# Kernel optimization log

Hardware: AMD Instinct MI355X
Metric: run time of the kernel (lower is better)

Reference implementation:

```python
import jax, jax.numpy as jnp
import numpy as np

B, S, H = 2, 2048, 2048
NH, DH = 16, 128
T, L = 8, 64
FF = 4 * H
SCALE = DH ** -0.5
EPS = 1e-5


def _ln(x, g, b):
    m = jnp.mean(x, axis=-1, keepdims=True)
    v = jnp.mean(jnp.square(x - m), axis=-1, keepdims=True)
    return (x - m) * jax.lax.rsqrt(v + EPS) * g + b


def setup_inputs() -> dict:
    key = jax.random.key(0)
    ks = jax.random.split(key, 10)
    def w(k, shape):
        return jax.random.normal(k, shape, jnp.float32) * (shape[0] ** -0.5)
    return {
        "hidden_states": jax.random.normal(ks[0], (B, S, H), jnp.float32),
        "image_embeds": jax.random.normal(ks[1], (B, T, L, H), jnp.float32),
        "media_locations": jax.random.randint(ks[2], (B, S), 0, 2).astype(bool),
        "Wq": w(ks[3], (H, NH * DH)),
        "Wk": w(ks[4], (H, NH * DH)),
        "Wv": w(ks[5], (H, NH * DH)),
        "Wo": w(ks[6], (NH * DH, H)),
        "ln_attn_g": jnp.ones((H,), jnp.float32),
        "ln_attn_b": jnp.zeros((H,), jnp.float32),
        "ln_ff_g": jnp.ones((H,), jnp.float32),
        "ln_ff_b": jnp.zeros((H,), jnp.float32),
        "W1": w(ks[7], (H, FF)),
        "b1": jnp.zeros((FF,), jnp.float32),
        "W2": w(ks[8], (FF, H)),
        "b2": jnp.zeros((H,), jnp.float32),
        # nonzero gates so the attention/ffn branches carry gradient signal
        "gamma_attn": jnp.full((1,), 0.1, jnp.float32),
        "gamma_ff": jnp.full((1,), 0.1, jnp.float32),
    }


def reference(hidden_states, image_embeds, media_locations,
              Wq, Wk, Wv, Wo, ln_attn_g, ln_attn_b, ln_ff_g, ln_ff_b,
              W1, b1, W2, b2, gamma_attn, gamma_ff):
    b, s, d = hidden_states.shape
    x = _ln(hidden_states, ln_attn_g, ln_attn_b)
    kv = image_embeds.reshape(b, -1, d)              # [B, T*L, D]
    q = (x @ Wq).reshape(b, s, NH, DH)               # [B, S, H, Dh]
    k = (kv @ Wk).reshape(b, -1, NH, DH)             # [B, KV, H, Dh]
    v = (kv @ Wv).reshape(b, -1, NH, DH)
    scores = jnp.einsum('bqhd,bkhd->bhqk', q, k) * SCALE
    # mask is per query row: rows with media_locations==False are fully masked.
    # Use large-finite neg (not -inf) to avoid NaN rows; those rows are zeroed below anyway.
    neg = jnp.finfo(scores.dtype).min
    scores = jnp.where(media_locations[:, None, :, None], scores, neg)
    attn = jax.nn.softmax(scores, axis=-1)
    out = jnp.einsum('bhqk,bkhd->bqhd', attn, v).reshape(b, s, NH * DH) @ Wo
    gated = jnp.tanh(gamma_attn) * out * media_locations[..., None].astype(hidden_states.dtype)
    x = hidden_states + gated
    ff = jax.nn.gelu(_ln(x, ln_ff_g, ln_ff_b) @ W1 + b1, approximate=False) @ W2 + b2
    return x + jnp.tanh(gamma_ff) * ff
```

## Files before the change

### kernel.cpp

```cpp
#include <hip/hip_runtime.h>
#include <math.h>
#include <stdint.h>

typedef __bf16 bf16;
typedef __bf16 bf16x8 __attribute__((ext_vector_type(8)));
typedef __bf16 bf16x4 __attribute__((ext_vector_type(4)));
typedef float f32x4 __attribute__((ext_vector_type(4)));

#define DEV __device__ __forceinline__

DEV void g2l16(void* lds, const void* g) {
    __builtin_amdgcn_global_load_lds(
        (const __attribute__((address_space(1))) uint32_t*)g,
        (__attribute__((address_space(3))) uint32_t*)lds,
        16, 0, 0);
}

DEV float gelu_fast(float x) {
    float u = -1.5957691216f * __builtin_fmaf(0.044715f * x, x * x, x);
    return x * __builtin_amdgcn_rcpf(1.f + __expf(u));
}

DEV uint8_t to_fp8(float x) {
    return (uint8_t)(__builtin_amdgcn_cvt_pk_fp8_f32(x, x, 0, false) & 0xff);
}

DEV void xcd_swizzle(int& bx, int& by, int& bz) {
    int gx = gridDim.x, gy = gridDim.y, gz = gridDim.z;
    int nwg = gx * gy * gz;
    if (nwg & 7) return;
    long flat = ((long)bz * gy + by) * gx + bx;
    long q = nwg >> 3;
    long sw = (flat & 7) * q + (flat >> 3);
    bx = (int)(sw % gx);
    long t = sw / gx;
    by = (int)(t % gy);
    bz = (int)(t / gy);
}

template <int EPI, typename TC>
__global__ __launch_bounds__(256)
void gemm_bt(const bf16* __restrict__ A, const bf16* __restrict__ Bt, TC* __restrict__ C,
             int K, int lda, int ldb, int ldc,
             long sAo, long sAi, long sBo, long sBi, long sCo, long sCi, int zInner,
             float alpha,
             const float* __restrict__ resid,
             const float* __restrict__ gamma,
             const int* __restrict__ mask)
{
    int bx = blockIdx.x, by = blockIdx.y, bz = blockIdx.z;
    xcd_swizzle(bx, by, bz);

    int zo = bz / zInner, zi = bz % zInner;
    A  += (long)zo * sAo + (long)zi * sAi;
    Bt += (long)zo * sBo + (long)zi * sBi;
    long cOff = (long)zo * sCo + (long)zi * sCi;

    int tileN = bx * 128, tileM = by * 128;

    __shared__ bf16 As[8192];
    __shared__ bf16 Bs[8192];

    int tid = threadIdx.x;
    int wave = tid >> 6, lane = tid & 63, quad = lane >> 4, l15 = lane & 15;
    int wm = (wave >> 1) * 64, wn = (wave & 1) * 64;

    f32x4 acc[4][4] = {};

    for (int k0 = 0; k0 < K; k0 += 64) {
#pragma unroll
        for (int r = 0; r < 4; ++r) {
            int c = r * 256 + tid;
            int kc = c >> 7, row = c & 127;
            g2l16(&As[c * 8], A + (long)(tileM + row) * lda + (k0 + kc * 8));
            g2l16(&Bs[c * 8], Bt + (long)(tileN + row) * ldb + (k0 + kc * 8));
        }
        __syncthreads();
#pragma unroll
        for (int ks = 0; ks < 2; ++ks) {
            bf16x8 af[4], bq[4];
#pragma unroll
            for (int i = 0; i < 4; ++i) {
                af[i] = *(const bf16x8*)&As[((ks * 4 + quad) * 128 + wm + i * 16 + l15) * 8];
                bq[i] = *(const bf16x8*)&Bs[((ks * 4 + quad) * 128 + wn + i * 16 + l15) * 8];
            }
#pragma unroll
            for (int mi = 0; mi < 4; ++mi)
#pragma unroll
                for (int ni = 0; ni < 4; ++ni)
                    acc[mi][ni] = __builtin_amdgcn_mfma_f32_16x16x32_bf16(
                        af[mi], bq[ni], acc[mi][ni], 0, 0, 0);
        }
        __syncthreads();
    }

    float gscale = 0.f;
    if (EPI == 2) gscale = tanhf(gamma[0]);

#pragma unroll
    for (int mi = 0; mi < 4; ++mi) {
#pragma unroll
        for (int r = 0; r < 4; ++r) {
            int gm = tileM + wm + mi * 16 + quad * 4 + r;
            float rowmask = 1.f;
            if (EPI == 2) rowmask = mask[gm] ? 1.f : 0.f;
#pragma unroll
            for (int ni = 0; ni < 4; ++ni) {
                int gn = tileN + wn + ni * 16 + l15;
                float v = acc[mi][ni][r] * alpha;
                float r0;
                if (EPI == 0) {
                    r0 = v;
                } else {
                    float h = resid[(long)gm * ldc + gn];
                    r0 = h + gscale * v * rowmask;
                }
                C[cOff + (long)gm * ldc + gn] = (TC)r0;
            }
        }
    }
}

__global__ __launch_bounds__(256)
void gemm_fp8(const uint8_t* __restrict__ A, const uint8_t* __restrict__ Bt,
              float* __restrict__ C, int K, int lda, int ldb, int ldc, float alpha,
              const float* __restrict__ resid,
              const float* __restrict__ bias,
              const float* __restrict__ gamma)
{
    int bx = blockIdx.x, by = blockIdx.y, bz = blockIdx.z;
    xcd_swizzle(bx, by, bz);

    int tileN = bx * 128, tileM = by * 128;

    __shared__ uint8_t As[16384];
    __shared__ uint8_t Bs[16384];

    int tid = threadIdx.x;
    int wave = tid >> 6, lane = tid & 63, quad = lane >> 4, l15 = lane & 15;
    int wm = (wave >> 1) * 64, wn = (wave & 1) * 64;

    f32x4 acc[4][4] = {};

    for (int k0 = 0; k0 < K; k0 += 128) {
#pragma unroll
        for (int r = 0; r < 4; ++r) {
            int c = r * 256 + tid;
            int kc = c >> 7, row = c & 127;
            g2l16(&As[c * 16], A + (long)(tileM + row) * lda + (k0 + kc * 16));
            g2l16(&Bs[c * 16], Bt + (long)(tileN + row) * ldb + (k0 + kc * 16));
        }
        __syncthreads();
#pragma unroll
        for (int ks = 0; ks < 4; ++ks) {
            int kc16 = ks * 2 + (quad >> 1);
            int boff = (quad & 1) * 8;
            long af[4], bq[4];
#pragma unroll
            for (int i = 0; i < 4; ++i) {
                af[i] = *(const long*)&As[(kc16 * 128 + wm + i * 16 + l15) * 16 + boff];
                bq[i] = *(const long*)&Bs[(kc16 * 128 + wn + i * 16 + l15) * 16 + boff];
            }
#pragma unroll
            for (int mi = 0; mi < 4; ++mi)
#pragma unroll
                for (int ni = 0; ni < 4; ++ni)
                    acc[mi][ni] = __builtin_amdgcn_mfma_f32_16x16x32_fp8_fp8(
                        af[mi], bq[ni], acc[mi][ni], 0, 0, 0);
        }
        __syncthreads();
    }

    float gscale = tanhf(gamma[0]);
    float bb[4];
#pragma unroll
    for (int ni = 0; ni < 4; ++ni)
        bb[ni] = bias[tileN + wn + ni * 16 + l15];

#pragma unroll
    for (int mi = 0; mi < 4; ++mi) {
#pragma unroll
        for (int r = 0; r < 4; ++r) {
            int gm = tileM + wm + mi * 16 + quad * 4 + r;
#pragma unroll
            for (int ni = 0; ni < 4; ++ni) {
                int gn = tileN + wn + ni * 16 + l15;
                float h = resid[(long)gm * ldc + gn];
                C[(long)gm * ldc + gn] = h + gscale * (acc[mi][ni][r] * alpha + bb[ni]);
            }
        }
    }
}

__global__ __launch_bounds__(512, 2)
void gemm256_h1(const bf16* __restrict__ A, const bf16* __restrict__ Bt,
                uint8_t* __restrict__ C, int K, int lda, int ldb, int ldc,
                const float* __restrict__ bias)
{
    __shared__ bf16 lds[3][2][8192];

    int bx = blockIdx.x, by = blockIdx.y, bz = blockIdx.z;
    xcd_swizzle(bx, by, bz);

    int tid = threadIdx.x;
    int wave = tid >> 6, lane = tid & 63, quad = lane >> 4, l15 = lane & 15;
    int wm = (wave >> 2) * 128, wn = (wave & 3) * 64;
    int tileN = bx * 256, tileM = by * 256;

    int c0 = tid, c1 = 512 + tid;
    int kc0 = c0 >> 8, row0 = c0 & 255;
    int kc1 = c1 >> 8, row1 = c1 & 255;
    const bf16* A0 = A + (long)(tileM + row0) * lda + kc0 * 8;
    const bf16* A1 = A + (long)(tileM + row1) * lda + kc1 * 8;
    const bf16* B0 = Bt + (long)(tileN + row0) * ldb + kc0 * 8;
    const bf16* B1 = Bt + (long)(tileN + row1) * ldb + kc1 * 8;

    f32x4 acc[8][4] = {};

    int aoff = (quad * 256 + wm + l15) * 8;
    int boff = (quad * 256 + wn + l15) * 8;

    auto stage = [&](int t, int b) {
        int k0 = t * 32;
        g2l16(&lds[b][0][c0 * 8], A0 + k0);
        g2l16(&lds[b][0][c1 * 8], A1 + k0);
        g2l16(&lds[b][1][c0 * 8], B0 + k0);
        g2l16(&lds[b][1][c1 * 8], B1 + k0);
    };

    stage(0, 0);
    stage(1, 1);

    int T = K >> 5;
    int cb = 0;
    for (int t = 0; t < T; ++t) {
        int nb = cb + 2; if (nb >= 3) nb -= 3;
        stage(t + 2, nb);

        asm volatile("s_waitcnt vmcnt(8)\n\ts_barrier" ::: "memory");

        const bf16* pA = &lds[cb][0][0];
        const bf16* pB = &lds[cb][1][0];
        bf16x8 af[8], bq[4];
#pragma unroll
        for (int mi = 0; mi < 8; ++mi)
            af[mi] = *(const bf16x8*)&pA[aoff + mi * 128];
#pragma unroll
        for (int ni = 0; ni < 4; ++ni)
            bq[ni] = *(const bf16x8*)&pB[boff + ni * 128];

        __builtin_amdgcn_s_setprio(1);
#pragma unroll
        for (int mi = 0; mi < 8; ++mi)
#pragma unroll
            for (int ni = 0; ni < 4; ++ni)
                acc[mi][ni] = __builtin_amdgcn_mfma_f32_16x16x32_bf16(
                    af[mi], bq[ni], acc[mi][ni], 0, 0, 0);
        __builtin_amdgcn_s_setprio(0);

        asm volatile("s_barrier" ::: "memory");
        cb = (cb == 2) ? 0 : cb + 1;
    }

    float bb[4];
#pragma unroll
    for (int ni = 0; ni < 4; ++ni)
        bb[ni] = bias[tileN + wn + ni * 16 + l15];

#pragma unroll
    for (int mi = 0; mi < 8; ++mi) {
#pragma unroll
        for (int r = 0; r < 4; ++r) {
            int gm = tileM + wm + mi * 16 + quad * 4 + r;
#pragma unroll
            for (int ni = 0; ni < 4; ++ni) {
                int gn = tileN + wn + ni * 16 + l15;
                float x = acc[mi][ni][r] + bb[ni];
                C[(long)gm * ldc + gn] = to_fp8(8.f * gelu_fast(x));
            }
        }
    }
}

__global__ __launch_bounds__(256)
void ln_k(const float* __restrict__ x, const float* __restrict__ g, const float* __restrict__ b,
          bf16* __restrict__ out)
{
    long row = blockIdx.x;
    int tid = threadIdx.x;
    int wave = tid >> 6, lane = tid & 63;
    const float* px = x + row * 2048 + tid * 8;

    float4 a = *(const float4*)px;
    float4 c = *(const float4*)(px + 4);
    float f[8] = {a.x, a.y, a.z, a.w, c.x, c.y, c.z, c.w};

    float s = 0.f, s2 = 0.f;
#pragma unroll
    for (int j = 0; j < 8; ++j) { s += f[j]; s2 += f[j] * f[j]; }
    for (int o = 32; o; o >>= 1) { s += __shfl_xor(s, o, 64); s2 += __shfl_xor(s2, o, 64); }

    __shared__ float red[8];
    if (lane == 0) { red[wave] = s; red[4 + wave] = s2; }
    __syncthreads();
    s  = red[0] + red[1] + red[2] + red[3];
    s2 = red[4] + red[5] + red[6] + red[7];

    float mean = s * (1.f / 2048.f);
    float var  = s2 * (1.f / 2048.f) - mean * mean;
    float rstd = rsqrtf(var + 1e-5f);

    int col = tid * 8;
    bf16x8 o8;
#pragma unroll
    for (int j = 0; j < 8; ++j)
        o8[j] = (bf16)((f[j] - mean) * rstd * g[col + j] + b[col + j]);
    *(bf16x8*)(out + row * 2048 + tid * 8) = o8;
}

__global__ __launch_bounds__(256)
void softmax512(bf16* __restrict__ s)
{
    long row = (long)blockIdx.x * 4 + (threadIdx.x >> 6);
    int lane = threadIdx.x & 63;
    bf16* p = s + row * 512 + lane * 8;
    bf16x8 v = *(const bf16x8*)p;
    float f[8], mx = -1e30f;
#pragma unroll
    for (int j = 0; j < 8; ++j) { f[j] = (float)v[j]; mx = fmaxf(mx, f[j]); }
    for (int o = 32; o; o >>= 1) mx = fmaxf(mx, __shfl_xor(mx, o, 64));
    float sum = 0.f;
#pragma unroll
    for (int j = 0; j < 8; ++j) { f[j] = __expf(f[j] - mx); sum += f[j]; }
    for (int o = 32; o; o >>= 1) sum += __shfl_xor(sum, o, 64);
    float r = 1.f / sum;
    bf16x8 o8;
#pragma unroll
    for (int j = 0; j < 8; ++j) o8[j] = (bf16)(f[j] * r);
    *(bf16x8*)p = o8;
}

__global__ __launch_bounds__(256)
void transpose_cvt(const float* __restrict__ in, bf16* __restrict__ out, int ldi, int ldo)
{
    __shared__ float t[64][33];
    int tx = threadIdx.x & 31, ty = threadIdx.x >> 5;
    int n0 = blockIdx.x * 32, m0 = blockIdx.y * 64;
#pragma unroll
    for (int i = 0; i < 8; ++i)
        t[ty + i * 8][tx] = in[(long)(m0 + ty + i * 8) * ldi + n0 + tx];
    __syncthreads();
    int wx = threadIdx.x & 15, wy = threadIdx.x >> 4;
#pragma unroll
    for (int j = 0; j < 2; ++j) {
        int n = wy + j * 16;
        bf16x4 v;
        v[0] = (bf16)t[4 * wx + 0][n];
        v[1] = (bf16)t[4 * wx + 1][n];
        v[2] = (bf16)t[4 * wx + 2][n];
        v[3] = (bf16)t[4 * wx + 3][n];
        *(bf16x4*)(out + (long)(n0 + n) * ldo + m0 + 4 * wx) = v;
    }
}

__global__ __launch_bounds__(256)
void transpose_cvt8(const float* __restrict__ in, uint8_t* __restrict__ out,
                    int ldi, int ldo, float scale)
{
    __shared__ float t[64][33];
    int tx = threadIdx.x & 31, ty = threadIdx.x >> 5;
    int n0 = blockIdx.x * 32, m0 = blockIdx.y * 64;
#pragma unroll
    for (int i = 0; i < 8; ++i)
        t[ty + i * 8][tx] = in[(long)(m0 + ty + i * 8) * ldi + n0 + tx];
    __syncthreads();
    int wx = threadIdx.x & 15, wy = threadIdx.x >> 4;
#pragma unroll
    for (int j = 0; j < 2; ++j) {
        int n = wy + j * 16;
        int p = __builtin_amdgcn_cvt_pk_fp8_f32(
            scale * t[4 * wx + 0][n], scale * t[4 * wx + 1][n], 0, false);
        p = __builtin_amdgcn_cvt_pk_fp8_f32(
            scale * t[4 * wx + 2][n], scale * t[4 * wx + 3][n], p, true);
        *(int*)(out + (long)(n0 + n) * ldo + m0 + 4 * wx) = p;
    }
}

__global__ __launch_bounds__(256)
void transpose_k(const bf16* __restrict__ in, bf16* __restrict__ out,
                 int ldi, int ldo, long sIo, long sIi, long sOo, long sOi, int zInner)
{
    int z = blockIdx.z;
    in  += (long)(z / zInner) * sIo + (long)(z % zInner) * sIi;
    out += (long)(z / zInner) * sOo + (long)(z % zInner) * sOi;
    __shared__ bf16 t[32][33];
    int tx = threadIdx.x & 31, ty = threadIdx.x >> 5;
    int n0 = blockIdx.x * 32, m0 = blockIdx.y * 32;
#pragma unroll
    for (int i = 0; i < 4; ++i)
        t[ty + i * 8][tx] = in[(long)(m0 + ty + i * 8) * ldi + n0 + tx];
    __syncthreads();
#pragma unroll
    for (int i = 0; i < 4; ++i)
        out[(long)(n0 + ty + i * 8) * ldo + m0 + tx] = t[tx][ty + i * 8];
}

__global__ __launch_bounds__(256)
void cvt_k(const float* __restrict__ in, bf16* __restrict__ out)
{
    int i = (blockIdx.x * 256 + threadIdx.x) * 4;
    float4 v = *(const float4*)(in + i);
    out[i + 0] = (bf16)v.x;
    out[i + 1] = (bf16)v.y;
    out[i + 2] = (bf16)v.z;
    out[i + 3] = (bf16)v.w;
}

extern "C" void kernel_launch(void* const* d_in, const int* in_sizes, int n_in,
                              void* d_out, int out_size, void* d_ws, size_t ws_size,
                              hipStream_t stream)
{
    const float* hidden = (const float*)d_in[0];
    const float* image  = (const float*)d_in[1];
    const int*   media  = (const int*)d_in[2];
    const float* Wq = (const float*)d_in[3];
    const float* Wk = (const float*)d_in[4];
    const float* Wv = (const float*)d_in[5];
    const float* Wo = (const float*)d_in[6];
    const float* lag = (const float*)d_in[7];
    const float* lab = (const float*)d_in[8];
    const float* lfg = (const float*)d_in[9];
    const float* lfb = (const float*)d_in[10];
    const float* W1 = (const float*)d_in[11];
    const float* b1 = (const float*)d_in[12];
    const float* W2 = (const float*)d_in[13];
    const float* b2 = (const float*)d_in[14];
    const float* ga = (const float*)d_in[15];
    const float* gf = (const float*)d_in[16];
    float* out = (float*)d_out;

    char* ws = (char*)d_ws;
    const size_t MB = 1ull << 20;
    bf16* WqT  = (bf16*)(ws + 0);
    bf16* WkT  = (bf16*)(ws + 8 * MB);
    bf16* WvT  = (bf16*)(ws + 16 * MB);
    bf16* WoT  = (bf16*)(ws + 24 * MB);
    bf16* W1T  = (bf16*)(ws + 0);
    uint8_t* W2T8 = (uint8_t*)(ws + 32 * MB);
    bf16* xln  = (bf16*)(ws + 32 * MB);
    bf16* q    = (bf16*)(ws + 48 * MB);
    bf16* kbuf = (bf16*)(ws + 64 * MB);
    bf16* vbuf = (bf16*)(ws + 68 * MB);
    bf16* vt   = (bf16*)(ws + 72 * MB);
    bf16* imgb = (bf16*)(ws + 76 * MB);
    bf16* sc   = (bf16*)(ws + 80 * MB);
    uint8_t* h1f8 = (uint8_t*)(ws + 80 * MB);
    float* x2  = (float*)(ws + 144 * MB);

    const float SCALE = 0.08838834764831845f;
    const float A8 = 8.f, B8 = 64.f;
    dim3 blk(256);

    transpose_cvt<<<dim3(64, 32, 1), blk, 0, stream>>>(Wq, WqT, 2048, 2048);
    transpose_cvt<<<dim3(64, 32, 1), blk, 0, stream>>>(Wk, WkT, 2048, 2048);
    transpose_cvt<<<dim3(64, 32, 1), blk, 0, stream>>>(Wv, WvT, 2048, 2048);
    transpose_cvt<<<dim3(64, 32, 1), blk, 0, stream>>>(Wo, WoT, 2048, 2048);
    cvt_k<<<2048, blk, 0, stream>>>(image, imgb);

    ln_k<<<4096, blk, 0, stream>>>(hidden, lag, lab, xln);

    gemm_bt<0, bf16><<<dim3(16, 32, 1), blk, 0, stream>>>(
        xln, WqT, q, 2048, 2048, 2048, 2048, 0, 0, 0, 0, 0, 0, 1, 1.f,
        nullptr, nullptr, nullptr);

    gemm_bt<0, bf16><<<dim3(16, 8, 2), blk, 0, stream>>>(
        imgb, WkT, kbuf, 2048, 2048, 2048, 2048,
        0, 0, 0, 4194304, 0, 2097152, 2, 1.f,
        nullptr, nullptr, nullptr);

    transpose_k<<<dim3(4, 16, 32), blk, 0, stream>>>(
        vbuf, vt, 2048, 512, 1048576, 128, 1048576, 65536, 16);

    gemm_bt<0, bf16><<<dim3(4, 16, 32), blk, 0, stream>>>(
        q, kbuf, sc, 128, 2048, 2048, 512,
        4194304, 128, 1048576, 128, 16777216, 1048576, 16, SCALE,
        nullptr, nullptr, nullptr);

    softmax512<<<16384, blk, 0, stream>>>(sc);

    gemm_bt<0, bf16><<<dim3(1, 16, 32), blk, 0, stream>>>(
        sc, vt, q, 512, 512, 512, 2048,
        16777216, 1048576, 1048576, 65536, 4194304, 128, 16, 1.f,
        nullptr, nullptr, nullptr);

    gemm_bt<2, float><<<dim3(16, 32, 1), blk, 0, stream>>>(
        q, WoT, x2, 2048, 2048, 2048, 2048, 0, 0, 0, 0, 0, 0, 1, 1.f,
        hidden, ga, media);

    transpose_cvt<<<dim3(256, 32, 1), blk, 0, stream>>>(W1, W1T, 8192, 2048);

    ln_k<<<4096, blk, 0, stream>>>(x2, lfg, lfb, xln);

    gemm256_h1<<<dim3(32, 16, 1), dim3(512), 0, stream>>>(
        xln, W1T, h1f8, 2048, 2048, 2048, 8192, b1);

    transpose_cvt8<<<dim3(64, 128, 1), blk, 0, stream>>>(W2, W2T8, 2048, 8192, B8);

    gemm_fp8<<<dim3(16, 32, 1), blk, 0, stream>>>(
        h1f8, W2T8, out, 8192, 8192, 8192, 2048, 1.f / (A8 * B8),
        x2, b2, gf);
}
```

Baseline: 916.5 us.

## Move Q, O, and FF1 projections to FP8 GEMMs with scaled quantization

Converts the Q projection, output projection, and first FFN matmul from bf16 to FP8 MFMA. LayerNorm now writes scaled FP8 directly, the attention-value GEMM emits FP8 for the output projection, and the weights are transposed into FP8 with a scale of 64. The tuned 256-tile bf16 FFN1 kernel is removed in favour of the generic 128-tile FP8 kernel, which gains gelu, residual, and mask epilogue variants. This aims to halve operand bandwidth and double MFMA throughput, at the cost of extra quantization error and giving up the triple-buffered pipeline of the removed kernel.

New measurement: 797.2 us. 1.15x faster.

```diff
diff --git a/kernel.cpp b/kernel.cpp
--- a/kernel.cpp
+++ b/kernel.cpp
@@ -43,10 +43,7 @@
 void gemm_bt(const bf16* __restrict__ A, const bf16* __restrict__ Bt, TC* __restrict__ C,
              int K, int lda, int ldb, int ldc,
              long sAo, long sAi, long sBo, long sBi, long sCo, long sCi, int zInner,
-             float alpha,
-             const float* __restrict__ resid,
-             const float* __restrict__ gamma,
-             const int* __restrict__ mask)
+             float alpha)
 {
     int bx = blockIdx.x, by = blockIdx.y, bz = blockIdx.z;
     xcd_swizzle(bx, by, bz);
@@ -94,39 +91,33 @@
         __syncthreads();
     }
 
-    float gscale = 0.f;
-    if (EPI == 2) gscale = tanhf(gamma[0]);
-
 #pragma unroll
     for (int mi = 0; mi < 4; ++mi) {
 #pragma unroll
         for (int r = 0; r < 4; ++r) {
             int gm = tileM + wm + mi * 16 + quad * 4 + r;
-            float rowmask = 1.f;
-            if (EPI == 2) rowmask = mask[gm] ? 1.f : 0.f;
 #pragma unroll
             for (int ni = 0; ni < 4; ++ni) {
                 int gn = tileN + wn + ni * 16 + l15;
                 float v = acc[mi][ni][r] * alpha;
-                float r0;
                 if (EPI == 0) {
-                    r0 = v;
+                    C[cOff + (long)gm * ldc + gn] = (TC)v;
                 } else {
-                    float h = resid[(long)gm * ldc + gn];
-                    r0 = h + gscale * v * rowmask;
+                    C[cOff + (long)gm * ldc + gn] = (TC)to_fp8(16.f * v);
                 }
-                C[cOff + (long)gm * ldc + gn] = (TC)r0;
             }
         }
     }
 }
 
+template <int EPI, typename TC>
 __global__ __launch_bounds__(256)
 void gemm_fp8(const uint8_t* __restrict__ A, const uint8_t* __restrict__ Bt,
-              float* __restrict__ C, int K, int lda, int ldb, int ldc, float alpha,
+              TC* __restrict__ C, int K, int lda, int ldb, int ldc, float alpha,
               const float* __restrict__ resid,
               const float* __restrict__ bias,
-              const float* __restrict__ gamma)
+              const float* __restrict__ gamma,
+              const int* __restrict__ mask)
 {
     int bx = blockIdx.x, by = blockIdx.y, bz = blockIdx.z;
     xcd_swizzle(bx, by, bz);
@@ -171,120 +162,45 @@
         __syncthreads();
     }
 
-    float gscale = tanhf(gamma[0]);
-    float bb[4];
-#pragma unroll
-    for (int ni = 0; ni < 4; ++ni)
-        bb[ni] = bias[tileN + wn + ni * 16 + l15];
+    float gscale = 0.f;
+    if (EPI == 2 || EPI == 3) gscale = tanhf(gamma[0]);
+    float bb[4] = {};
+    if (EPI == 1 || EPI == 3) {
+#pragma unroll
+        for (int ni = 0; ni < 4; ++ni)
+            bb[ni] = bias[tileN + wn + ni * 16 + l15];
+    }
 
 #pragma unroll
     for (int mi = 0; mi < 4; ++mi) {
 #pragma unroll
         for (int r = 0; r < 4; ++r) {
             int gm = tileM + wm + mi * 16 + quad * 4 + r;
+            float rowmask = 1.f;
+            if (EPI == 2) rowmask = mask[gm] ? 1.f : 0.f;
 #pragma unroll
             for (int ni = 0; ni < 4; ++ni) {
                 int gn = tileN + wn + ni * 16 + l15;
-                float h = resid[(long)gm * ldc + gn];
-                C[(long)gm * ldc + gn] = h + gscale * (acc[mi][ni][r] * alpha + bb[ni]);
+                float v = acc[mi][ni][r] * alpha;
+                if (EPI == 0) {
+                    C[(long)gm * ldc + gn] = (TC)v;
+                } else if (EPI == 1) {
+                    C[(long)gm * ldc + gn] = (TC)to_fp8(8.f * gelu_fast(v + bb[ni]));
+                } else if (EPI == 2) {
+                    float h = resid[(long)gm * ldc + gn];
+                    C[(long)gm * ldc + gn] = (TC)(h + gscale * v * rowmask);
+                } else {
+                    float h = resid[(long)gm * ldc + gn];
+                    C[(long)gm * ldc + gn] = (TC)(h + gscale * (v + bb[ni]));
+                }
             }
         }
     }
 }
 
-__global__ __launch_bounds__(512, 2)
-void gemm256_h1(const bf16* __restrict__ A, const bf16* __restrict__ Bt,
-                uint8_t* __restrict__ C, int K, int lda, int ldb, int ldc,
-                const float* __restrict__ bias)
-{
-    __shared__ bf16 lds[3][2][8192];
-
-    int bx = blockIdx.x, by = blockIdx.y, bz = blockIdx.z;
-    xcd_swizzle(bx, by, bz);
-
-    int tid = threadIdx.x;
-    int wave = tid >> 6, lane = tid & 63, quad = lane >> 4, l15 = lane & 15;
-    int wm = (wave >> 2) * 128, wn = (wave & 3) * 64;
-    int tileN = bx * 256, tileM = by * 256;
-
-    int c0 = tid, c1 = 512 + tid;
-    int kc0 = c0 >> 8, row0 = c0 & 255;
-    int kc1 = c1 >> 8, row1 = c1 & 255;
-    const bf16* A0 = A + (long)(tileM + row0) * lda + kc0 * 8;
-    const bf16* A1 = A + (long)(tileM + row1) * lda + kc1 * 8;
-    const bf16* B0 = Bt + (long)(tileN + row0) * ldb + kc0 * 8;
-    const bf16* B1 = Bt + (long)(tileN + row1) * ldb + kc1 * 8;
-
-    f32x4 acc[8][4] = {};
-
-    int aoff = (quad * 256 + wm + l15) * 8;
-    int boff = (quad * 256 + wn + l15) * 8;
-
-    auto stage = [&](int t, int b) {
-        int k0 = t * 32;
-        g2l16(&lds[b][0][c0 * 8], A0 + k0);
-        g2l16(&lds[b][0][c1 * 8], A1 + k0);
-        g2l16(&lds[b][1][c0 * 8], B0 + k0);
-        g2l16(&lds[b][1][c1 * 8], B1 + k0);
-    };
-
-    stage(0, 0);
-    stage(1, 1);
-
-    int T = K >> 5;
-    int cb = 0;
-    for (int t = 0; t < T; ++t) {
-        int nb = cb + 2; if (nb >= 3) nb -= 3;
-        stage(t + 2, nb);
-
-        asm volatile("s_waitcnt vmcnt(8)\n\ts_barrier" ::: "memory");
-
-        const bf16* pA = &lds[cb][0][0];
-        const bf16* pB = &lds[cb][1][0];
-        bf16x8 af[8], bq[4];
-#pragma unroll
-        for (int mi = 0; mi < 8; ++mi)
-            af[mi] = *(const bf16x8*)&pA[aoff + mi * 128];
-#pragma unroll
-        for (int ni = 0; ni < 4; ++ni)
-            bq[ni] = *(const bf16x8*)&pB[boff + ni * 128];
-
-        __builtin_amdgcn_s_setprio(1);
-#pragma unroll
-        for (int mi = 0; mi < 8; ++mi)
-#pragma unroll
-            for (int ni = 0; ni < 4; ++ni)
-                acc[mi][ni] = __builtin_amdgcn_mfma_f32_16x16x32_bf16(
-                    af[mi], bq[ni], acc[mi][ni], 0, 0, 0);
-        __builtin_amdgcn_s_setprio(0);
-
-        asm volatile("s_barrier" ::: "memory");
-        cb = (cb == 2) ? 0 : cb + 1;
-    }
-
-    float bb[4];
-#pragma unroll
-    for (int ni = 0; ni < 4; ++ni)
-        bb[ni] = bias[tileN + wn + ni * 16 + l15];
-
-#pragma unroll
-    for (int mi = 0; mi < 8; ++mi) {
-#pragma unroll
-        for (int r = 0; r < 4; ++r) {
-            int gm = tileM + wm + mi * 16 + quad * 4 + r;
-#pragma unroll
-            for (int ni = 0; ni < 4; ++ni) {
-                int gn = tileN + wn + ni * 16 + l15;
-                float x = acc[mi][ni][r] + bb[ni];
-                C[(long)gm * ldc + gn] = to_fp8(8.f * gelu_fast(x));
-            }
-        }
-    }
-}
-
-__global__ __launch_bounds__(256)
-void ln_k(const float* __restrict__ x, const float* __restrict__ g, const float* __restrict__ b,
-          bf16* __restrict__ out)
+__global__ __launch_bounds__(256)
+void ln8_k(const float* __restrict__ x, const float* __restrict__ g, const float* __restrict__ b,
+           uint8_t* __restrict__ out)
 {
     long row = blockIdx.x;
     int tid = threadIdx.x;
@@ -311,11 +227,15 @@
     float rstd = rsqrtf(var + 1e-5f);
 
     int col = tid * 8;
-    bf16x8 o8;
+    float o[8];
 #pragma unroll
     for (int j = 0; j < 8; ++j)
-        o8[j] = (bf16)((f[j] - mean) * rstd * g[col + j] + b[col + j]);
-    *(bf16x8*)(out + row * 2048 + tid * 8) = o8;
+        o[j] = 16.f * ((f[j] - mean) * rstd * g[col + j] + b[col + j]);
+    int p0 = __builtin_amdgcn_cvt_pk_fp8_f32(o[0], o[1], 0, false);
+    p0     = __builtin_amdgcn_cvt_pk_fp8_f32(o[2], o[3], p0, true);
+    int p1 = __builtin_amdgcn_cvt_pk_fp8_f32(o[4], o[5], 0, false);
+    p1     = __builtin_amdgcn_cvt_pk_fp8_f32(o[6], o[7], p1, true);
+    *(int2*)(out + row * 2048 + tid * 8) = make_int2(p0, p1);
 }
 
 __global__ __launch_bounds__(256)
@@ -441,72 +361,73 @@
 
     char* ws = (char*)d_ws;
     const size_t MB = 1ull << 20;
-    bf16* WqT  = (bf16*)(ws + 0);
-    bf16* WkT  = (bf16*)(ws + 8 * MB);
-    bf16* WvT  = (bf16*)(ws + 16 * MB);
-    bf16* WoT  = (bf16*)(ws + 24 * MB);
-    bf16* W1T  = (bf16*)(ws + 0);
+    uint8_t* WqT8 = (uint8_t*)(ws + 0);
+    uint8_t* WoT8 = (uint8_t*)(ws + 4 * MB);
+    bf16*    WkT  = (bf16*)(ws + 8 * MB);
+    bf16*    WvT  = (bf16*)(ws + 16 * MB);
+    uint8_t* W1T8 = (uint8_t*)(ws + 0);
+    uint8_t* xln8 = (uint8_t*)(ws + 32 * MB);
     uint8_t* W2T8 = (uint8_t*)(ws + 32 * MB);
-    bf16* xln  = (bf16*)(ws + 32 * MB);
-    bf16* q    = (bf16*)(ws + 48 * MB);
-    bf16* kbuf = (bf16*)(ws + 64 * MB);
-    bf16* vbuf = (bf16*)(ws + 68 * MB);
-    bf16* vt   = (bf16*)(ws + 72 * MB);
-    bf16* imgb = (bf16*)(ws + 76 * MB);
-    bf16* sc   = (bf16*)(ws + 80 * MB);
+    bf16*    q    = (bf16*)(ws + 48 * MB);
+    uint8_t* ao8  = (uint8_t*)(ws + 48 * MB);
+    uint8_t* ln28 = (uint8_t*)(ws + 48 * MB);
+    bf16*    kbuf = (bf16*)(ws + 64 * MB);
+    bf16*    vbuf = (bf16*)(ws + 68 * MB);
+    bf16*    vt   = (bf16*)(ws + 72 * MB);
+    bf16*    imgb = (bf16*)(ws + 76 * MB);
+    bf16*    sc   = (bf16*)(ws + 80 * MB);
     uint8_t* h1f8 = (uint8_t*)(ws + 80 * MB);
-    float* x2  = (float*)(ws + 144 * MB);
+    float*   x2   = (float*)(ws + 144 * MB);
 
     const float SCALE = 0.08838834764831845f;
-    const float A8 = 8.f, B8 = 64.f;
+    const float INV1024 = 1.f / 1024.f;
+    const float INV512  = 1.f / 512.f;
     dim3 blk(256);
 
-    transpose_cvt<<<dim3(64, 32, 1), blk, 0, stream>>>(Wq, WqT, 2048, 2048);
-    transpose_cvt<<<dim3(64, 32, 1), blk, 0, stream>>>(Wk, WkT, 2048, 2048);
-    transpose_cvt<<<dim3(64, 32, 1), blk, 0, stream>>>(Wv, WvT, 2048, 2048);
-    transpose_cvt<<<dim3(64, 32, 1), blk, 0, stream>>>(Wo, WoT, 2048, 2048);
+    transpose_cvt8<<<dim3(64, 32, 1), blk, 0, stream>>>(Wq, WqT8, 2048, 2048, 64.f);
+    transpose_cvt <<<dim3(64, 32, 1), blk, 0, stream>>>(Wk, WkT, 2048, 2048);
+    transpose_cvt <<<dim3(64, 32, 1), blk, 0, stream>>>(Wv, WvT, 2048, 2048);
+    transpose_cvt8<<<dim3(64, 32, 1), blk, 0, stream>>>(Wo, WoT8, 2048, 2048, 64.f);
     cvt_k<<<2048, blk, 0, stream>>>(image, imgb);
 
-    ln_k<<<4096, blk, 0, stream>>>(hidden, lag, lab, xln);
-
-    gemm_bt<0, bf16><<<dim3(16, 32, 1), blk, 0, stream>>>(
-        xln, WqT, q, 2048, 2048, 2048, 2048, 0, 0, 0, 0, 0, 0, 1, 1.f,
-        nullptr, nullptr, nullptr);
+    ln8_k<<<4096, blk, 0, stream>>>(hidden, lag, lab, xln8);
+
+    gemm_fp8<0, bf16><<<dim3(16, 32, 1), blk, 0, stream>>>(
+        xln8, WqT8, q, 2048, 2048, 2048, 2048, INV1024,
+        nullptr, nullptr, nullptr, nullptr);
 
     gemm_bt<0, bf16><<<dim3(16, 8, 2), blk, 0, stream>>>(
         imgb, WkT, kbuf, 2048, 2048, 2048, 2048,
-        0, 0, 0, 4194304, 0, 2097152, 2, 1.f,
-        nullptr, nullptr, nullptr);
+        0, 0, 0, 4194304, 0, 2097152, 2, 1.f);
 
     transpose_k<<<dim3(4, 16, 32), blk, 0, stream>>>(
         vbuf, vt, 2048, 512, 1048576, 128, 1048576, 65536, 16);
 
     gemm_bt<0, bf16><<<dim3(4, 16, 32), blk, 0, stream>>>(
         q, kbuf, sc, 128, 2048, 2048, 512,
-        4194304, 128, 1048576, 128, 16777216, 1048576, 16, SCALE,
-        nullptr, nullptr, nullptr);
+        4194304, 128, 1048576, 128, 16777216, 1048576, 16, SCALE);
 
     softmax512<<<16384, blk, 0, stream>>>(sc);
 
-    gemm_bt<0, bf16><<<dim3(1, 16, 32), blk, 0, stream>>>(
-        sc, vt, q, 512, 512, 512, 2048,
-        16777216, 1048576, 1048576, 65536, 4194304, 128, 16, 1.f,
-        nullptr, nullptr, nullptr);
-
-    gemm_bt<2, float><<<dim3(16, 32, 1), blk, 0, stream>>>(
-        q, WoT, x2, 2048, 2048, 2048, 2048, 0, 0, 0, 0, 0, 0, 1, 1.f,
-        hidden, ga, media);
-
-    transpose_cvt<<<dim3(256, 32, 1), blk, 0, stream>>>(W1, W1T, 8192, 2048);
-
-    ln_k<<<4096, blk, 0, stream>>>(x2, lfg, lfb, xln);
-
-    gemm256_h1<<<dim3(32, 16, 1), dim3(512), 0, stream>>>(
-        xln, W1T, h1f8, 2048, 2048, 2048, 8192, b1);
-
-    transpose_cvt8<<<dim3(64, 128, 1), blk, 0, stream>>>(W2, W2T8, 2048, 8192, B8);
-
-    gemm_fp8<<<dim3(16, 32, 1), blk, 0, stream>>>(
-        h1f8, W2T8, out, 8192, 8192, 8192, 2048, 1.f / (A8 * B8),
-        x2, b2, gf);
-}
+    gemm_bt<4, uint8_t><<<dim3(1, 16, 32), blk, 0, stream>>>(
+        sc, vt, ao8, 512, 512, 512, 2048,
+        16777216, 1048576, 1048576, 65536, 4194304, 128, 16, 1.f);
+
+    gemm_fp8<2, float><<<dim3(16, 32, 1), blk, 0, stream>>>(
+        ao8, WoT8, x2, 2048, 2048, 2048, 2048, INV1024,
+        hidden, nullptr, ga, media);
+
+    transpose_cvt8<<<dim3(256, 32, 1), blk, 0, stream>>>(W1, W1T8, 8192, 2048, 64.f);
+
+    ln8_k<<<4096, blk, 0, stream>>>(x2, lfg, lfb, ln28);
+
+    gemm_fp8<1, uint8_t><<<dim3(64, 32, 1), blk, 0, stream>>>(
+        ln28, W1T8, h1f8, 2048, 2048, 2048, 8192, INV1024,
+        nullptr, b1, nullptr, nullptr);
+
+    transpose_cvt8<<<dim3(64, 128, 1), blk, 0, stream>>>(W2, W2T8, 2048, 8192, 64.f);
+
+    gemm_fp8<3, float><<<dim3(16, 32, 1), blk, 0, stream>>>(
+        h1f8, W2T8, out, 8192, 8192, 8192, 2048, INV512,
+        x2, b2, gf, nullptr);
+}
```
